# Performance work log

Measured on AMD Instinct MI355X. Metric: run time of the kernel, lower is better.

Reference implementation:

```python
import jax, jax.numpy as jnp
import numpy as np

B, L, D = 256, 64, 1024          # batch trees, leaves, embedding dim
V, C = 50000, 500                # vocab, num categories
N = 2 * L - 1                    # total tree nodes
S = L - 1                        # compose steps


def _left_branching_tree():
    # step i combines (prev internal or leaf0, leaf i+1) -> internal slot L+i
    ci = np.zeros((S, 3), dtype=np.int32)
    ci[0] = [0, 1, L]
    for i in range(1, S):
        ci[i] = [L + i - 1, i + 1, L + i]
    return ci


def setup_inputs() -> dict:
    key = jax.random.key(0)
    k1, k2, k3 = jax.random.split(key, 3)
    leaf_content_id = jax.random.randint(k1, (B, L), 0, V, dtype=jnp.int32)
    content_mask = jnp.ones((B, L), dtype=jnp.int32)
    composition_info = jnp.asarray(np.broadcast_to(_left_branching_tree(), (B, S, 3)).copy())
    emb_weight = jax.random.normal(k2, (V, D), jnp.float32) * 0.1
    lin_w = jax.random.normal(k3, (C, D), jnp.float32) * (1.0 / np.sqrt(D))
    lin_b = jnp.zeros((C,), jnp.float32)
    return {
        'leaf_content_id': leaf_content_id,
        'content_mask': content_mask,
        'composition_info': composition_info,
        'emb_weight': emb_weight,
        'lin_w': lin_w,
        'lin_b': lin_b,
    }


def circular_correlation(a, b):
    # corr(a,b)[k] = sum_i a[i] * b[(i+k) mod d], via FFT; result unit-normalized
    fa = jnp.fft.rfft(a, axis=-1)
    fb = jnp.fft.rfft(b, axis=-1)
    c = jnp.fft.irfft(jnp.conj(fa) * fb, n=a.shape[-1], axis=-1)
    return c / (jnp.linalg.norm(c, axis=-1, keepdims=True) + 1e-6)


def reference(leaf_content_id, content_mask, composition_info, emb_weight, lin_w, lin_b):
    # --- embed_leaf_nodes ---
    leaf_vec = emb_weight[leaf_content_id]                       # [B, L, D]
    vec = jnp.zeros((B, N, D), emb_weight.dtype)
    vec = vec.at[:, :L, :].set(jnp.where(content_mask[..., None] > 0, leaf_vec, 0.0))
    vec = vec / (jnp.linalg.norm(vec, axis=-1, keepdims=True) + 1e-6)
    # --- compose: sequential gather/correlate/scatter over tree steps ---
    barange = jnp.arange(B)
    def step(v, info):                                           # info: [B, 3]
        lv = v[barange, info[:, 0]]                              # [B, D]
        rv = v[barange, info[:, 1]]
        comp = circular_correlation(lv, rv)
        v = v.at[barange, info[:, 2]].set(comp)
        return v, None
    vec, _ = jax.lax.scan(step, vec, jnp.swapaxes(composition_info, 0, 1))
    # --- classifier ---
    logits = jnp.einsum('bnd,cd->bnc', vec, lin_w) + lin_b       # [B, N, C]
    return jax.nn.sigmoid(logits)
```

## Files before the change

### kernel.cpp

```cpp
#include <hip/hip_runtime.h>


#define BATCH 256
#define LLEN 64
#define DDIM 1024
#define NNODE 127
#define NSTEP 63
#define NCLS 500
#define NCLSP 512

#define PAD(i) ((i) + ((i) >> 5))

typedef __attribute__((ext_vector_type(8))) __bf16 bf16x8_t;
typedef __attribute__((ext_vector_type(4))) float f32x4_t;

__device__ __forceinline__ short f2bf(float f) {
  union { float f; unsigned u; } v; v.f = f;
  unsigned r = v.u + 0x7FFFu + ((v.u >> 16) & 1u);
  return (short)(r >> 16);
}

__global__ __launch_bounds__(256) void leaf_init(
    const int* __restrict__ ids, const int* __restrict__ cmask,
    const float* __restrict__ emb, float* __restrict__ vec) {
  const int n = blockIdx.x, b = blockIdx.y, t = threadIdx.x;
  float* dst = vec + ((size_t)b * NNODE + n) * DDIM + 4 * t;
  if (n >= LLEN) {
    float4 z = make_float4(0.f, 0.f, 0.f, 0.f);
    *(float4*)dst = z;
    return;
  }
  __shared__ float sred[4];
  const int id = ids[b * LLEN + n];
  const int m = cmask[b * LLEN + n];
  float4 v = make_float4(0.f, 0.f, 0.f, 0.f);
  if (m > 0) v = *(const float4*)(emb + (size_t)id * DDIM + 4 * t);
  float ss = v.x * v.x + v.y * v.y + v.z * v.z + v.w * v.w;
#pragma unroll
  for (int off = 32; off > 0; off >>= 1) ss += __shfl_xor(ss, off);
  if ((t & 63) == 0) sred[t >> 6] = ss;
  __syncthreads();
  const float tot = sred[0] + sred[1] + sred[2] + sred[3];
  const float rn = 1.f / (sqrtf(tot) + 1e-6f);
  v.x *= rn; v.y *= rn; v.z *= rn; v.w *= rn;
  *(float4*)dst = v;
}

__global__ __launch_bounds__(256) void conv_w(const float* __restrict__ w,
                                              short* __restrict__ wb) {
  const int i = (blockIdx.x * 256 + threadIdx.x) * 4;
  short4 o;
  if (i < NCLS * DDIM) {
    float4 f = *(const float4*)(w + i);
    o.x = f2bf(f.x); o.y = f2bf(f.y); o.z = f2bf(f.z); o.w = f2bf(f.w);
  } else {
    o.x = 0; o.y = 0; o.z = 0; o.w = 0;
  }
  *(short4*)(wb + i) = o;
}

__global__ __launch_bounds__(512) void tree_scan(const int* __restrict__ comp,
                                                 float* __restrict__ vec) {
  __shared__ float lvs[DDIM];
  __shared__ float rvs[2112];
  __shared__ float cstore[DDIM];
  __shared__ float partial[8 * 1056];
  __shared__ int infoS[NSTEP * 3];
  __shared__ float redS[8];
  const int b = blockIdx.x, t = threadIdx.x;
  const int jc = t >> 6, k0 = (t & 63) * 16, j0 = jc * 128;
  float* vb = vec + (size_t)b * NNODE * DDIM;
  if (t < NSTEP * 3) infoS[t] = comp[b * NSTEP * 3 + t];
  __syncthreads();
  int prev = -1;
  for (int s = 0; s < NSTEP; ++s) {
    const int i0 = infoS[3 * s], i1 = infoS[3 * s + 1], i2 = infoS[3 * s + 2];
    {
      const float* sl = (i0 == prev) ? cstore : (vb + (size_t)i0 * DDIM);
      lvs[t] = sl[t];
      lvs[t + 512] = sl[t + 512];
      const float* sr = (i1 == prev) ? cstore : (vb + (size_t)i1 * DDIM);
      const float a0 = sr[t], a1 = sr[t + 512];
      rvs[PAD(t)] = a0; rvs[PAD(t + 512)] = a1;
      rvs[PAD(t + 1024)] = a0; rvs[PAD(t + 1536)] = a1;
    }
    __syncthreads();
    float w[16], acc[16];
#pragma unroll
    for (int r = 0; r < 16; ++r) {
      w[r] = rvs[PAD(j0 + k0 + r)];
      acc[r] = 0.f;
    }
    for (int jb = 0; jb < 8; ++jb) {
      const int jbase = j0 + jb * 16;
#pragma unroll
      for (int jj = 0; jj < 16; ++jj) {
        const float a = lvs[jbase + jj];
#pragma unroll
        for (int r = 0; r < 16; ++r) acc[r] += a * w[(jj + r) & 15];
        w[jj] = rvs[PAD(jbase + jj + 16 + k0)];
      }
    }
#pragma unroll
    for (int r = 0; r < 16; ++r) partial[jc * 1056 + PAD(k0) + r] = acc[r];
    __syncthreads();
    const int ka = t, kb = t + 512;
    float c0 = 0.f, c1 = 0.f;
#pragma unroll
    for (int j = 0; j < 8; ++j) {
      c0 += partial[j * 1056 + PAD(ka)];
      c1 += partial[j * 1056 + PAD(kb)];
    }
    float ssq = c0 * c0 + c1 * c1;
#pragma unroll
    for (int off = 32; off > 0; off >>= 1) ssq += __shfl_xor(ssq, off);
    if ((t & 63) == 0) redS[t >> 6] = ssq;
    __syncthreads();
    const float tot = redS[0] + redS[1] + redS[2] + redS[3] +
                      redS[4] + redS[5] + redS[6] + redS[7];
    const float rn = 1.f / (sqrtf(tot) + 1e-6f);
    const float o0 = c0 * rn, o1 = c1 * rn;
    float* dst = vb + (size_t)i2 * DDIM;
    dst[ka] = o0; dst[kb] = o1;
    cstore[ka] = o0; cstore[kb] = o1;
    prev = i2;
    __syncthreads();
  }
}

__global__ __launch_bounds__(256) void gemm_out(
    const float* __restrict__ A, const short* __restrict__ Bw,
    const float* __restrict__ bias, float* __restrict__ out) {
  __shared__ short As[128 * 64];
  __shared__ short Bs[128 * 64];
  const int t = threadIdx.x;
  const int trow = blockIdx.x * 128, tcol = blockIdx.y * 128;
  const int wv = t >> 6, lane = t & 63;
  const int wr = wv >> 1, wc = wv & 1;
  const int lr = lane & 15, kg = lane >> 4;
  f32x4_t acc[4][4];
  const f32x4_t zz = {0.f, 0.f, 0.f, 0.f};
#pragma unroll
  for (int i = 0; i < 4; ++i)
#pragma unroll
    for (int j = 0; j < 4; ++j) acc[i][j] = zz;

  for (int kt = 0; kt < 16; ++kt) {
    const int kof = kt * 64;
#pragma unroll
    for (int q = 0; q < 8; ++q) {
      const int c = t + q * 256;
      const int row = c >> 4, colf = (c & 15) * 4;
      float4 f = *(const float4*)(A + (size_t)(trow + row) * DDIM + kof + colf);
      short4 p;
      p.x = f2bf(f.x); p.y = f2bf(f.y); p.z = f2bf(f.z); p.w = f2bf(f.w);
      *(short4*)&As[row * 64 + colf] = p;
    }
#pragma unroll
    for (int q = 0; q < 4; ++q) {
      const int c = t + q * 256;
      const int row = c >> 3, coli = (c & 7) * 8;
      *(int4*)&Bs[row * 64 + coli] =
          *(const int4*)(Bw + (size_t)(tcol + row) * DDIM + kof + coli);
    }
    __syncthreads();
#pragma unroll
    for (int kk = 0; kk < 2; ++kk) {
      bf16x8_t af[4], bfr[4];
#pragma unroll
      for (int mi = 0; mi < 4; ++mi)
        af[mi] = *(const bf16x8_t*)&As[(wr * 64 + mi * 16 + lr) * 64 + kk * 32 + kg * 8];
#pragma unroll
      for (int ni = 0; ni < 4; ++ni)
        bfr[ni] = *(const bf16x8_t*)&Bs[(wc * 64 + ni * 16 + lr) * 64 + kk * 32 + kg * 8];
#pragma unroll
      for (int mi = 0; mi < 4; ++mi)
#pragma unroll
        for (int ni = 0; ni < 4; ++ni)
          acc[mi][ni] = __builtin_amdgcn_mfma_f32_16x16x32_bf16(
              af[mi], bfr[ni], acc[mi][ni], 0, 0, 0);
    }
    __syncthreads();
  }
  const int mbase = trow + wr * 64;
  const int nbase = tcol + wc * 64;
#pragma unroll
  for (int ni = 0; ni < 4; ++ni) {
    const int col = nbase + ni * 16 + lr;
    if (col < NCLS) {
      const float bb = bias[col];
#pragma unroll
      for (int mi = 0; mi < 4; ++mi) {
#pragma unroll
        for (int vv = 0; vv < 4; ++vv) {
          const int row = mbase + mi * 16 + kg * 4 + vv;
          const float x = acc[mi][ni][vv] + bb;
          out[(size_t)row * NCLS + col] = 1.f / (1.f + __expf(-x));
        }
      }
    }
  }
}

extern "C" void kernel_launch(void* const* d_in, const int* in_sizes, int n_in,
                              void* d_out, int out_size, void* d_ws, size_t ws_size,
                              hipStream_t stream) {
  const int* ids = (const int*)d_in[0];
  const int* cmask = (const int*)d_in[1];
  const int* comp = (const int*)d_in[2];
  const float* emb = (const float*)d_in[3];
  const float* linw = (const float*)d_in[4];
  const float* linb = (const float*)d_in[5];
  float* out = (float*)d_out;

  char* ws = (char*)d_ws;
  float* vecf = (float*)ws;
  short* linwb = (short*)(ws + (size_t)BATCH * NNODE * DDIM * 4);

  leaf_init<<<dim3(NNODE, BATCH), 256, 0, stream>>>(ids, cmask, emb, vecf);
  conv_w<<<(NCLSP * DDIM) / 1024, 256, 0, stream>>>(linw, linwb);
  tree_scan<<<BATCH, 512, 0, stream>>>(comp, vecf);
  gemm_out<<<dim3((BATCH * NNODE) / 128, NCLSP / 128), 256, 0, stream>>>(
      vecf, linwb, linb, out);
}
```

Measured before the change: 927.1 us.

## Vectorize tree_scan correlation with blocked LDS layout and forward composed vector

Replaces the scalar padded LDS layout in the tree_scan correlation with a blocked, padded layout (SB) that allows 128-bit LDS loads of both operands and of the partial sums. The right operand is stored once and accessed through a double-buffered 8-vector register window, instead of as a duplicated circular copy. The composed vector is written directly into lvs when the next step's left child is the node just produced, skipping a reload. The aim is fewer LDS instructions and bank conflicts in the sequential per-step inner loop, at the cost of more complex indexing and higher register pressure.

```diff
diff --git a/kernel.cpp b/kernel.cpp
--- a/kernel.cpp
+++ b/kernel.cpp
@@ -9,7 +9,7 @@
 #define NCLS 500
 #define NCLSP 512
 
-#define PAD(i) ((i) + ((i) >> 5))
+#define SB(bi) ((((bi) >> 3) * 160) + (((bi) & 7) * 20))
 
 typedef __attribute__((ext_vector_type(8))) __bf16 bf16x8_t;
 typedef __attribute__((ext_vector_type(4))) float f32x4_t;
@@ -61,55 +61,89 @@
 
 __global__ __launch_bounds__(512) void tree_scan(const int* __restrict__ comp,
                                                  float* __restrict__ vec) {
-  __shared__ float lvs[DDIM];
-  __shared__ float rvs[2112];
-  __shared__ float cstore[DDIM];
-  __shared__ float partial[8 * 1056];
+  __shared__ __align__(16) float lvs[DDIM];
+  __shared__ __align__(16) float rvs[2560];
+  __shared__ __align__(16) float cstore[DDIM];
+  __shared__ __align__(16) float part[8 * 1280];
   __shared__ int infoS[NSTEP * 3];
   __shared__ float redS[8];
   const int b = blockIdx.x, t = threadIdx.x;
-  const int jc = t >> 6, k0 = (t & 63) * 16, j0 = jc * 128;
+  const int lane = t & 63, jc = t >> 6;
+  const int j0 = jc * 128;
+  const int bi0 = jc * 8 + lane;
   float* vb = vec + (size_t)b * NNODE * DDIM;
   if (t < NSTEP * 3) infoS[t] = comp[b * NSTEP * 3 + t];
   __syncthreads();
   int prev = -1;
   for (int s = 0; s < NSTEP; ++s) {
     const int i0 = infoS[3 * s], i1 = infoS[3 * s + 1], i2 = infoS[3 * s + 2];
+    if (i0 != prev) {
+      const float2 lq = *(const float2*)(vb + (size_t)i0 * DDIM + 2 * t);
+      *(float2*)&lvs[2 * t] = lq;
+    }
     {
-      const float* sl = (i0 == prev) ? cstore : (vb + (size_t)i0 * DDIM);
-      lvs[t] = sl[t];
-      lvs[t + 512] = sl[t + 512];
-      const float* sr = (i1 == prev) ? cstore : (vb + (size_t)i1 * DDIM);
-      const float a0 = sr[t], a1 = sr[t + 512];
-      rvs[PAD(t)] = a0; rvs[PAD(t + 512)] = a1;
-      rvs[PAD(t + 1024)] = a0; rvs[PAD(t + 1536)] = a1;
-    }
-    __syncthreads();
-    float w[16], acc[16];
-#pragma unroll
-    for (int r = 0; r < 16; ++r) {
-      w[r] = rvs[PAD(j0 + k0 + r)];
-      acc[r] = 0.f;
-    }
+      f32x4_t rq;
+      if (i1 == prev) rq = *(const f32x4_t*)&cstore[4 * (t & 255)];
+      else rq = *(const f32x4_t*)(vb + (size_t)i1 * DDIM + 4 * (t & 255));
+      *(f32x4_t*)&rvs[SB(t >> 2) + (t & 3) * 4] = rq;
+    }
+    __syncthreads();
+    f32x4_t W8[8], acc4[4], av[4];
+    {
+      const float* w0 = &rvs[SB(bi0)];
+      const float* w1 = &rvs[SB(bi0 + 1)];
+      W8[0] = *(const f32x4_t*)(w0);
+      W8[1] = *(const f32x4_t*)(w0 + 4);
+      W8[2] = *(const f32x4_t*)(w0 + 8);
+      W8[3] = *(const f32x4_t*)(w0 + 12);
+      W8[4] = *(const f32x4_t*)(w1);
+      W8[5] = *(const f32x4_t*)(w1 + 4);
+      W8[6] = *(const f32x4_t*)(w1 + 8);
+      W8[7] = *(const f32x4_t*)(w1 + 12);
+    }
+    const f32x4_t zz = {0.f, 0.f, 0.f, 0.f};
+    acc4[0] = zz; acc4[1] = zz; acc4[2] = zz; acc4[3] = zz;
+#pragma unroll
     for (int jb = 0; jb < 8; ++jb) {
       const int jbase = j0 + jb * 16;
+      av[0] = *(const f32x4_t*)&lvs[jbase];
+      av[1] = *(const f32x4_t*)&lvs[jbase + 4];
+      av[2] = *(const f32x4_t*)&lvs[jbase + 8];
+      av[3] = *(const f32x4_t*)&lvs[jbase + 12];
 #pragma unroll
       for (int jj = 0; jj < 16; ++jj) {
-        const float a = lvs[jbase + jj];
-#pragma unroll
-        for (int r = 0; r < 16; ++r) acc[r] += a * w[(jj + r) & 15];
-        w[jj] = rvs[PAD(jbase + jj + 16 + k0)];
+        const float a = av[jj >> 2][jj & 3];
+#pragma unroll
+        for (int r = 0; r < 16; ++r) {
+          const int x = (jj + r + 16 * jb) & 31;
+          acc4[r >> 2][r & 3] += a * W8[x >> 2][x & 3];
+        }
       }
-    }
-#pragma unroll
-    for (int r = 0; r < 16; ++r) partial[jc * 1056 + PAD(k0) + r] = acc[r];
+      if (jb < 7) {
+        const float* ns = &rvs[SB(bi0 + jb + 2)];
+        const int s0 = (jb & 1) ? 4 : 0;
+        W8[s0 + 0] = *(const f32x4_t*)(ns);
+        W8[s0 + 1] = *(const f32x4_t*)(ns + 4);
+        W8[s0 + 2] = *(const f32x4_t*)(ns + 8);
+        W8[s0 + 3] = *(const f32x4_t*)(ns + 12);
+      }
+    }
+    {
+      float* pw = &part[jc * 1280 + SB(lane)];
+      *(f32x4_t*)(pw) = acc4[0];
+      *(f32x4_t*)(pw + 4) = acc4[1];
+      *(f32x4_t*)(pw + 8) = acc4[2];
+      *(f32x4_t*)(pw + 12) = acc4[3];
+    }
     __syncthreads();
     const int ka = t, kb = t + 512;
+    const int ba = ka >> 4, oa = ka & 15;
+    const int bb = kb >> 4, ob = kb & 15;
     float c0 = 0.f, c1 = 0.f;
 #pragma unroll
     for (int j = 0; j < 8; ++j) {
-      c0 += partial[j * 1056 + PAD(ka)];
-      c1 += partial[j * 1056 + PAD(kb)];
+      c0 += part[j * 1280 + SB(ba) + oa];
+      c1 += part[j * 1280 + SB(bb) + ob];
     }
     float ssq = c0 * c0 + c1 * c1;
 #pragma unroll
@@ -123,6 +157,9 @@
     float* dst = vb + (size_t)i2 * DDIM;
     dst[ka] = o0; dst[kb] = o1;
     cstore[ka] = o0; cstore[kb] = o1;
+    if (s + 1 < NSTEP && infoS[3 * (s + 1)] == i2) {
+      lvs[ka] = o0; lvs[kb] = o1;
+    }
     prev = i2;
     __syncthreads();
   }
```

New measurement: 760.6 us. 18.0% less time.
